# Optimization experiments

Measured on AMD Instinct MI355X. Metric: run time of the kernel, lower is better.

## Reference

```python
import jax, jax.numpy as jnp
import numpy as np

DIM = 3            # point feature dim (xyz)
POS_HID = 64       # pos_mlp hidden
ATTN_HID = DIM * 4 # attn_mlp hidden (mult=4)
N_NBR = 16         # points per group
GROUPS = 512       # groups per batch element
MLP_D = N_NBR * DIM  # 48


def setup_inputs() -> dict:
    key = jax.random.key(0)
    ks = jax.random.split(key, 20)
    B = 32
    s = lambda *sh: 1.0 / np.sqrt(sh[0])
    inp = {
        "original_points": jax.random.normal(ks[0], (B, GROUPS, DIM), jnp.float32),
        "data": jax.random.normal(ks[1], (B, GROUPS, N_NBR, DIM), jnp.float32),
        # PointTransformerLayer params
        "w_qkv": jax.random.normal(ks[2], (DIM, DIM * 3), jnp.float32) * s(DIM),
        "pos_w1": jax.random.normal(ks[3], (3, POS_HID), jnp.float32) * s(3),
        "pos_b1": jnp.zeros((POS_HID,), jnp.float32),
        "pos_w2": jax.random.normal(ks[4], (POS_HID, DIM), jnp.float32) * s(POS_HID),
        "pos_b2": jnp.zeros((DIM,), jnp.float32),
        "attn_w1": jax.random.normal(ks[5], (DIM, ATTN_HID), jnp.float32) * s(DIM),
        "attn_b1": jnp.zeros((ATTN_HID,), jnp.float32),
        "attn_w2": jax.random.normal(ks[6], (ATTN_HID, DIM), jnp.float32) * s(ATTN_HID),
        "attn_b2": jnp.zeros((DIM,), jnp.float32),
        # downstream MLP params
        "mlp_w1": jax.random.normal(ks[7], (MLP_D, MLP_D), jnp.float32) * s(MLP_D),
        "mlp_b1": jnp.zeros((MLP_D,), jnp.float32),
        "mlp_w2": jax.random.normal(ks[8], (MLP_D, MLP_D), jnp.float32) * s(MLP_D),
        "mlp_b2": jnp.zeros((MLP_D,), jnp.float32),
        "mlp_w3": jax.random.normal(ks[9], (MLP_D, 1), jnp.float32) * s(MLP_D),
        "mlp_b3": jnp.zeros((1,), jnp.float32),
    }
    return inp


def reference(original_points, data, w_qkv, pos_w1, pos_b1, pos_w2, pos_b2,
              attn_w1, attn_b1, attn_w2, attn_b2,
              mlp_w1, mlp_b1, mlp_w2, mlp_b2, mlp_w3, mlp_b3):
    B, G, n, d = data.shape
    x = data.reshape(B * G, n, d)          # (BG, n, 3)
    pos = x[:, :, :3]                       # pos == features here (f=3)

    # Point-transformer vector attention
    qkv = x @ w_qkv                          # (BG, n, 9)
    q, k, v = jnp.split(qkv, 3, axis=-1)
    rel_pos = pos[:, :, None, :] - pos[:, None, :, :]              # (BG, n, n, 3)
    rel_emb = jax.nn.relu(rel_pos @ pos_w1 + pos_b1) @ pos_w2 + pos_b2  # (BG, n, n, 3)
    qk_rel = q[:, :, None, :] - k[:, None, :, :]                   # (BG, n, n, 3)
    v_ij = v[:, None, :, :] + rel_emb                              # (BG, n, n, 3)
    sim = jax.nn.relu((qk_rel + rel_emb) @ attn_w1 + attn_b1) @ attn_w2 + attn_b2
    attn = jax.nn.softmax(sim, axis=-2)                            # softmax over j
    agg = jnp.einsum('bijd,bijd->bid', attn, v_ij)                 # (BG, n, 3)

    # regroup into (B, 512, 48) exactly as stack(split(512, dim=0))
    sa = agg.reshape(B, G, n * d)
    h = jax.nn.relu(sa @ mlp_w1 + mlp_b1)
    h = jax.nn.relu(h @ mlp_w2 + mlp_b2)
    return h @ mlp_w3 + mlp_b3              # (B, 512, 1)
```

## Files before the change

### kernel.cpp

```cpp
#include <hip/hip_runtime.h>


#define ASTRIDE 68

__global__ __launch_bounds__(256) void pt_main(
    const float* __restrict__ data,
    const float* __restrict__ wqkv,
    const float* __restrict__ pw1,
    const float* __restrict__ pb1,
    const float* __restrict__ pw2,
    const float* __restrict__ pb2,
    const float* __restrict__ aw1,
    const float* __restrict__ ab1,
    const float* __restrict__ aw2,
    const float* __restrict__ ab2,
    const float* __restrict__ mw1,
    const float* __restrict__ mb1,
    const float* __restrict__ mw2,
    const float* __restrict__ mb2,
    const float* __restrict__ mw3,
    const float* __restrict__ mb3,
    float* __restrict__ out)
{
    __shared__ float s_pos[48];
    __shared__ float s_q[48], s_k[48], s_v[48];
    __shared__ float s_sa[48], s_h1[48];
    __shared__ float a1[16 * ASTRIDE];
    __shared__ float a2[16 * ASTRIDE];

    const int g = blockIdx.x;
    const int t = threadIdx.x;

    if (t < 48) s_pos[t] = data[g * 48 + t];
    __syncthreads();

    if (t < 48) {
        const int sec = t >> 4, p = t & 15;
        const float x0 = s_pos[p*3+0], x1 = s_pos[p*3+1], x2 = s_pos[p*3+2];
        float* dst = (sec == 0) ? s_q : (sec == 1) ? s_k : s_v;
        #pragma unroll
        for (int c = 0; c < 3; ++c) {
            dst[p*3+c] = fmaf(x0, wqkv[0*9 + sec*3 + c],
                         fmaf(x1, wqkv[1*9 + sec*3 + c],
                         x2 * wqkv[2*9 + sec*3 + c]));
        }
    }

    {
        const int i  = t >> 4;
        const int hc = (t & 15) << 2;
        const float x0 = s_pos[i*3+0], x1 = s_pos[i*3+1], x2 = s_pos[i*3+2];
        float4 va, vb;
        #pragma unroll
        for (int c = 0; c < 4; ++c) {
            const int h = hc + c;
            const float s = fmaf(x0, pw1[h], fmaf(x1, pw1[64+h], x2 * pw1[128+h]));
            (&vb.x)[c] = s;
            (&va.x)[c] = s + pb1[h];
        }
        *(float4*)&a1[i * ASTRIDE + hc] = va;
        *(float4*)&a2[i * ASTRIDE + hc] = vb;
    }
    __syncthreads();

    const int i = t >> 4, j = t & 15;

    float e0 = pb2[0], e1 = pb2[1], e2 = pb2[2];
    #pragma unroll
    for (int c16 = 0; c16 < 16; ++c16) {
        const int h0 = c16 * 4;
        const float4 ai = *(const float4*)&a1[i * ASTRIDE + h0];
        const float4 aj = *(const float4*)&a2[j * ASTRIDE + h0];
        #pragma unroll
        for (int c = 0; c < 4; ++c) {
            const float hh = fmaxf((&ai.x)[c] - (&aj.x)[c], 0.0f);
            e0 = fmaf(hh, pw2[(h0+c)*3+0], e0);
            e1 = fmaf(hh, pw2[(h0+c)*3+1], e1);
            e2 = fmaf(hh, pw2[(h0+c)*3+2], e2);
        }
    }

    const float vi0 = s_v[j*3+0] + e0, vi1 = s_v[j*3+1] + e1, vi2 = s_v[j*3+2] + e2;
    const float si0 = s_q[i*3+0] - s_k[j*3+0] + e0;
    const float si1 = s_q[i*3+1] - s_k[j*3+1] + e1;
    const float si2 = s_q[i*3+2] - s_k[j*3+2] + e2;

    float m0 = ab2[0], m1 = ab2[1], m2 = ab2[2];
    #pragma unroll
    for (int gg = 0; gg < 12; ++gg) {
        float hg = fmaf(si0, aw1[gg], fmaf(si1, aw1[12+gg], fmaf(si2, aw1[24+gg], ab1[gg])));
        hg = fmaxf(hg, 0.0f);
        m0 = fmaf(hg, aw2[gg*3+0], m0);
        m1 = fmaf(hg, aw2[gg*3+1], m1);
        m2 = fmaf(hg, aw2[gg*3+2], m2);
    }

    float x0 = m0, x1 = m1, x2 = m2;
    #pragma unroll
    for (int mk = 1; mk < 16; mk <<= 1) {
        x0 = fmaxf(x0, __shfl_xor(x0, mk));
        x1 = fmaxf(x1, __shfl_xor(x1, mk));
        x2 = fmaxf(x2, __shfl_xor(x2, mk));
    }
    float p0 = __expf(m0 - x0), p1 = __expf(m1 - x1), p2 = __expf(m2 - x2);

    float n0 = p0 * vi0, n1 = p1 * vi1, n2 = p2 * vi2;
    float d0 = p0, d1 = p1, d2 = p2;
    #pragma unroll
    for (int mk = 1; mk < 16; mk <<= 1) {
        n0 += __shfl_xor(n0, mk);  d0 += __shfl_xor(d0, mk);
        n1 += __shfl_xor(n1, mk);  d1 += __shfl_xor(d1, mk);
        n2 += __shfl_xor(n2, mk);  d2 += __shfl_xor(d2, mk);
    }
    if (j == 0) {
        s_sa[i*3+0] = n0 / d0;
        s_sa[i*3+1] = n1 / d1;
        s_sa[i*3+2] = n2 / d2;
    }
    __syncthreads();

    if (t < 48) {
        float h1 = mb1[t];
        #pragma unroll
        for (int c = 0; c < 48; ++c) h1 = fmaf(s_sa[c], mw1[c*48+t], h1);
        s_h1[t] = fmaxf(h1, 0.0f);
    }
    __syncthreads();

    float fv = 0.0f;
    if (t < 48) {
        float h2 = mb2[t];
        #pragma unroll
        for (int c = 0; c < 48; ++c) h2 = fmaf(s_h1[c], mw2[c*48+t], h2);
        h2 = fmaxf(h2, 0.0f);
        fv = h2 * mw3[t];
    }
    if (t < 64) {
        #pragma unroll
        for (int mk = 1; mk < 64; mk <<= 1) fv += __shfl_xor(fv, mk);
        if (t == 0) out[g] = fv + mb3[0];
    }
}

extern "C" void kernel_launch(void* const* d_in, const int* in_sizes, int n_in,
                              void* d_out, int out_size, void* d_ws, size_t ws_size,
                              hipStream_t stream) {
    const float* data = (const float*)d_in[1];
    const int groups = out_size;

    pt_main<<<groups, 256, 0, stream>>>(
        data,
        (const float*)d_in[2],  (const float*)d_in[3],  (const float*)d_in[4],
        (const float*)d_in[5],  (const float*)d_in[6],  (const float*)d_in[7],
        (const float*)d_in[8],  (const float*)d_in[9],  (const float*)d_in[10],
        (const float*)d_in[11], (const float*)d_in[12], (const float*)d_in[13],
        (const float*)d_in[14], (const float*)d_in[15], (const float*)d_in[16],
        (float*)d_out);
}
```

Before: 156.6 us.

## Use packed fp16 dot2 for pos MLP and DPP softmax reductions

Stores the pos-MLP hidden activations and the second-layer weights as packed fp16 in shared memory. The per-pair 64-wide hidden loop now uses packed subtract, relu and fdot2 with fp32 accumulation, which cuts ALU and LDS traffic in the hottest loop. The softmax drops the max-subtraction pass, uses exp2 intrinsics, sums with DPP row rotations instead of shuffles, and replaces division with rcp. In exchange it loses precision from fp16 rounding, and without the max shift large logits could overflow.

```diff
diff --git a/kernel.cpp b/kernel.cpp
--- a/kernel.cpp
+++ b/kernel.cpp
@@ -1,7 +1,41 @@
 #include <hip/hip_runtime.h>
 
 
-#define ASTRIDE 68
+typedef _Float16 h2 __attribute__((ext_vector_type(2)));
+typedef _Float16 h8 __attribute__((ext_vector_type(8)));
+
+#define AH_STRIDE 36
+#define WP_STRIDE 36
+
+union H8U { h8 v; h2 p[4]; unsigned u[4]; };
+
+__device__ __forceinline__ h2 pkrtz(float a, float b) {
+    return __builtin_bit_cast(h2, __builtin_amdgcn_cvt_pkrtz(a, b));
+}
+
+#if __has_builtin(__builtin_amdgcn_fdot2)
+__device__ __forceinline__ float dot2acc(h2 a, h2 b, float c) {
+    return __builtin_amdgcn_fdot2(a, b, c, false);
+}
+#else
+__device__ __forceinline__ float dot2acc(h2 a, h2 b, float c) {
+    return fmaf((float)a.x, (float)b.x, fmaf((float)a.y, (float)b.y, c));
+}
+#endif
+
+__device__ __forceinline__ float dpp_add16(float x) {
+    float s = x;
+    int t;
+    t = __builtin_amdgcn_update_dpp(0, __builtin_bit_cast(int, s), 0x121, 0xf, 0xf, false);
+    s += __builtin_bit_cast(float, t);
+    t = __builtin_amdgcn_update_dpp(0, __builtin_bit_cast(int, s), 0x122, 0xf, 0xf, false);
+    s += __builtin_bit_cast(float, t);
+    t = __builtin_amdgcn_update_dpp(0, __builtin_bit_cast(int, s), 0x124, 0xf, 0xf, false);
+    s += __builtin_bit_cast(float, t);
+    t = __builtin_amdgcn_update_dpp(0, __builtin_bit_cast(int, s), 0x128, 0xf, 0xf, false);
+    s += __builtin_bit_cast(float, t);
+    return s;
+}
 
 __global__ __launch_bounds__(256) void pt_main(
     const float* __restrict__ data,
@@ -22,11 +56,12 @@
     const float* __restrict__ mb3,
     float* __restrict__ out)
 {
-    __shared__ float s_pos[48];
-    __shared__ float s_q[48], s_k[48], s_v[48];
-    __shared__ float s_sa[48], s_h1[48];
-    __shared__ float a1[16 * ASTRIDE];
-    __shared__ float a2[16 * ASTRIDE];
+    __shared__ __attribute__((aligned(16))) float s_pos[48];
+    __shared__ __attribute__((aligned(16))) float s_q[48], s_k[48], s_v[48];
+    __shared__ __attribute__((aligned(16))) float s_sa[48], s_h1[48];
+    __shared__ __attribute__((aligned(16))) unsigned s_a1h[16 * AH_STRIDE];
+    __shared__ __attribute__((aligned(16))) unsigned s_a2h[16 * AH_STRIDE];
+    __shared__ __attribute__((aligned(16))) unsigned s_wp[3 * WP_STRIDE];
 
     const int g = blockIdx.x;
     const int t = threadIdx.x;
@@ -47,19 +82,30 @@
     }
 
     {
-        const int i  = t >> 4;
+        const int ii = t >> 4;
         const int hc = (t & 15) << 2;
-        const float x0 = s_pos[i*3+0], x1 = s_pos[i*3+1], x2 = s_pos[i*3+2];
-        float4 va, vb;
+        const float x0 = s_pos[ii*3+0], x1 = s_pos[ii*3+1], x2 = s_pos[ii*3+2];
+        float s[4];
         #pragma unroll
         for (int c = 0; c < 4; ++c) {
             const int h = hc + c;
-            const float s = fmaf(x0, pw1[h], fmaf(x1, pw1[64+h], x2 * pw1[128+h]));
-            (&vb.x)[c] = s;
-            (&va.x)[c] = s + pb1[h];
+            s[c] = fmaf(x0, pw1[h], fmaf(x1, pw1[64+h], x2 * pw1[128+h]));
         }
-        *(float4*)&a1[i * ASTRIDE + hc] = va;
-        *(float4*)&a2[i * ASTRIDE + hc] = vb;
+        h2 a1p0 = pkrtz(s[0] + pb1[hc+0], s[1] + pb1[hc+1]);
+        h2 a1p1 = pkrtz(s[2] + pb1[hc+2], s[3] + pb1[hc+3]);
+        h2 a2p0 = pkrtz(s[0], s[1]);
+        h2 a2p1 = pkrtz(s[2], s[3]);
+        const int base = ii * AH_STRIDE + (hc >> 1);
+        s_a1h[base+0] = __builtin_bit_cast(unsigned, a1p0);
+        s_a1h[base+1] = __builtin_bit_cast(unsigned, a1p1);
+        s_a2h[base+0] = __builtin_bit_cast(unsigned, a2p0);
+        s_a2h[base+1] = __builtin_bit_cast(unsigned, a2p1);
+    }
+
+    if (t < 96) {
+        const int hp = t & 31, c = t >> 5;
+        h2 wpair = pkrtz(pw2[(2*hp)*3 + c], pw2[(2*hp+1)*3 + c]);
+        s_wp[c * WP_STRIDE + hp] = __builtin_bit_cast(unsigned, wpair);
     }
     __syncthreads();
 
@@ -67,16 +113,21 @@
 
     float e0 = pb2[0], e1 = pb2[1], e2 = pb2[2];
     #pragma unroll
-    for (int c16 = 0; c16 < 16; ++c16) {
-        const int h0 = c16 * 4;
-        const float4 ai = *(const float4*)&a1[i * ASTRIDE + h0];
-        const float4 aj = *(const float4*)&a2[j * ASTRIDE + h0];
-        #pragma unroll
-        for (int c = 0; c < 4; ++c) {
-            const float hh = fmaxf((&ai.x)[c] - (&aj.x)[c], 0.0f);
-            e0 = fmaf(hh, pw2[(h0+c)*3+0], e0);
-            e1 = fmaf(hh, pw2[(h0+c)*3+1], e1);
-            e2 = fmaf(hh, pw2[(h0+c)*3+2], e2);
+    for (int cc = 0; cc < 8; ++cc) {
+        H8U ai, aj, w0, w1, w2;
+        ai.v = *(const h8*)&s_a1h[i * AH_STRIDE + cc*4];
+        aj.v = *(const h8*)&s_a2h[j * AH_STRIDE + cc*4];
+        w0.v = *(const h8*)&s_wp[0 * WP_STRIDE + cc*4];
+        w1.v = *(const h8*)&s_wp[1 * WP_STRIDE + cc*4];
+        w2.v = *(const h8*)&s_wp[2 * WP_STRIDE + cc*4];
+        #pragma unroll
+        for (int m = 0; m < 4; ++m) {
+            h2 d = ai.p[m] - aj.p[m];
+            h2 z = {(_Float16)0, (_Float16)0};
+            h2 r = { d.x > z.x ? d.x : z.x, d.y > z.y ? d.y : z.y };
+            e0 = dot2acc(r, w0.p[m], e0);
+            e1 = dot2acc(r, w1.p[m], e1);
+            e2 = dot2acc(r, w2.p[m], e2);
         }
     }
 
@@ -95,27 +146,22 @@
         m2 = fmaf(hg, aw2[gg*3+2], m2);
     }
 
-    float x0 = m0, x1 = m1, x2 = m2;
-    #pragma unroll
-    for (int mk = 1; mk < 16; mk <<= 1) {
-        x0 = fmaxf(x0, __shfl_xor(x0, mk));
-        x1 = fmaxf(x1, __shfl_xor(x1, mk));
-        x2 = fmaxf(x2, __shfl_xor(x2, mk));
-    }
-    float p0 = __expf(m0 - x0), p1 = __expf(m1 - x1), p2 = __expf(m2 - x2);
-
-    float n0 = p0 * vi0, n1 = p1 * vi1, n2 = p2 * vi2;
-    float d0 = p0, d1 = p1, d2 = p2;
-    #pragma unroll
-    for (int mk = 1; mk < 16; mk <<= 1) {
-        n0 += __shfl_xor(n0, mk);  d0 += __shfl_xor(d0, mk);
-        n1 += __shfl_xor(n1, mk);  d1 += __shfl_xor(d1, mk);
-        n2 += __shfl_xor(n2, mk);  d2 += __shfl_xor(d2, mk);
-    }
+    const float L2E = 1.44269504f;
+    const float p0 = __builtin_amdgcn_exp2f(m0 * L2E);
+    const float p1 = __builtin_amdgcn_exp2f(m1 * L2E);
+    const float p2 = __builtin_amdgcn_exp2f(m2 * L2E);
+
+    const float n0 = dpp_add16(p0 * vi0);
+    const float n1 = dpp_add16(p1 * vi1);
+    const float n2 = dpp_add16(p2 * vi2);
+    const float d0 = dpp_add16(p0);
+    const float d1 = dpp_add16(p1);
+    const float d2 = dpp_add16(p2);
+
     if (j == 0) {
-        s_sa[i*3+0] = n0 / d0;
-        s_sa[i*3+1] = n1 / d1;
-        s_sa[i*3+2] = n2 / d2;
+        s_sa[i*3+0] = n0 * __builtin_amdgcn_rcpf(d0);
+        s_sa[i*3+1] = n1 * __builtin_amdgcn_rcpf(d1);
+        s_sa[i*3+2] = n2 * __builtin_amdgcn_rcpf(d2);
     }
     __syncthreads();
 
@@ -129,11 +175,11 @@
 
     float fv = 0.0f;
     if (t < 48) {
-        float h2 = mb2[t];
-        #pragma unroll
-        for (int c = 0; c < 48; ++c) h2 = fmaf(s_h1[c], mw2[c*48+t], h2);
-        h2 = fmaxf(h2, 0.0f);
-        fv = h2 * mw3[t];
+        float h2v = mb2[t];
+        #pragma unroll
+        for (int c = 0; c < 48; ++c) h2v = fmaf(s_h1[c], mw2[c*48+t], h2v);
+        h2v = fmaxf(h2v, 0.0f);
+        fv = h2v * mw3[t];
     }
     if (t < 64) {
         #pragma unroll
```

New measurement: 143.6 us. -8.3%, faster.
